# Optimization experiments

Hardware: AMD Instinct MI355X
Metric: run time of the kernel (lower is better)

Reference implementation:

```python
import jax, jax.numpy as jnp
import numpy as np

N_EMBD = 1024
N_HEAD = 16
HEAD_DIM = N_EMBD // N_HEAD


def setup_inputs() -> dict:
    key = jax.random.key(0)
    kx, kq, kk, kv, ko = jax.random.split(key, 5)
    B, T, C = 2, 2048, N_EMBD
    s = 1.0 / np.sqrt(C)
    return {
        "x": jax.random.normal(kx, (B, T, C), dtype=jnp.float32),
        "Wq": jax.random.normal(kq, (C, C), dtype=jnp.float32) * s,
        "Wk": jax.random.normal(kk, (C, C), dtype=jnp.float32) * s,
        "Wv": jax.random.normal(kv, (C, C), dtype=jnp.float32) * s,
        "Wo": jax.random.normal(ko, (C, C), dtype=jnp.float32) * s,
    }


def reference(x, Wq, Wk, Wv, Wo):
    B, T, C = x.shape
    H, D = N_HEAD, HEAD_DIM
    # projections (torch Linear: y = x @ W^T)
    q = (x @ Wq.T).reshape(B, T, H, D).transpose(0, 2, 1, 3)  # [B,H,T,D]
    k = (x @ Wk.T).reshape(B, T, H, D).transpose(0, 2, 1, 3)
    v = (x @ Wv.T).reshape(B, T, H, D).transpose(0, 2, 1, 3)
    scale = 1.0 / np.sqrt(D).astype(np.float32)
    scores = jnp.einsum("bhqd,bhkd->bhqk", q, k) * scale  # [B,H,T,T]
    causal = jnp.tril(jnp.ones((T, T), dtype=bool))
    scores = jnp.where(causal, scores, -jnp.inf)
    attn = jax.nn.softmax(scores, axis=-1)
    y = jnp.einsum("bhqk,bhkd->bhqd", attn, v)  # [B,H,T,D]
    y = y.transpose(0, 2, 1, 3).reshape(B, T, C)
    return y @ Wo.T
```

## Files before the change

### kernel.cpp

```cpp
#include <hip/hip_runtime.h>
#include <hip/hip_bf16.h>
#include <math.h>

#define SEQ   2048
#define CDIM  1024
#define NH    16
#define HD    64

#define K_SCALE 0.1803368801111204f

typedef __attribute__((ext_vector_type(8))) short bf16x8;
typedef __attribute__((ext_vector_type(4))) float f32x4;
typedef __attribute__((ext_vector_type(4))) short short4v;

__device__ __forceinline__ short f2bf(float f) {
  return (short)__builtin_bit_cast(unsigned short, __float2bfloat16(f));
}

__device__ __forceinline__ void glds16(const short* g, short* l) {
  __builtin_amdgcn_global_load_lds(
      (const __attribute__((address_space(1))) unsigned int*)g,
      (__attribute__((address_space(3))) unsigned int*)l, 16, 0, 0);
}

__global__ void cvt_all(const float* __restrict__ x,
                        const float* __restrict__ w0, const float* __restrict__ w1,
                        const float* __restrict__ w2, const float* __restrict__ w3,
                        short* __restrict__ xb,
                        short* __restrict__ d0, short* __restrict__ d1,
                        short* __restrict__ d2, short* __restrict__ d3) {
  const int y = blockIdx.y;
  const float* src;
  short* dst;
  float mult = 1.0f;
  int i = blockIdx.x * blockDim.x + threadIdx.x;
  if (y < 4) {
    src = (y == 0) ? w0 : (y == 1) ? w1 : (y == 2) ? w2 : w3;
    dst = (y == 0) ? d0 : (y == 1) ? d1 : (y == 2) ? d2 : d3;
    if (y == 1) mult = K_SCALE;
  } else {
    src = x;
    dst = xb;
    i += (y - 4) * 262144;
  }
  float4 v = reinterpret_cast<const float4*>(src)[i];
  short4v o;
  o.x = f2bf(v.x * mult); o.y = f2bf(v.y * mult);
  o.z = f2bf(v.z * mult); o.w = f2bf(v.w * mult);
  reinterpret_cast<short4v*>(dst)[i] = o;
}

template<int MODE, int BN>
__global__ __launch_bounds__(256)
void gemm_bt(const short* __restrict__ A,
             const short* __restrict__ W0, const short* __restrict__ W1, const short* __restrict__ W2,
             short* __restrict__ ob0, short* __restrict__ ob1, short* __restrict__ ob2,
             float* __restrict__ of)
{
  constexpr int K = CDIM;
  constexpr int NJF = BN / 32;
  const int z = (MODE == 0) ? blockIdx.z : 0;
  const short* W;
  short* outb = nullptr;
  if (MODE == 0) {
    W    = (z == 0) ? W0  : (z == 1) ? W1  : W2;
    outb = (z == 0) ? ob0 : (z == 1) ? ob1 : ob2;
  } else {
    W = W0;
  }
  const int m0 = blockIdx.y * 128;
  const int n0 = blockIdx.x * BN;

  __shared__ __align__(16) short As[128 * 32];
  __shared__ __align__(16) short Bs[BN * 32];

  const int tid  = threadIdx.x;
  const int lane = tid & 63;
  const int wid  = tid >> 6;
  const int wr   = wid >> 1;
  const int wc   = wid & 1;
  const int rl   = lane & 15;
  const int g    = lane >> 4;

  f32x4 acc[4][NJF];
#pragma unroll
  for (int i = 0; i < 4; ++i)
#pragma unroll
    for (int j = 0; j < NJF; ++j)
      acc[i][j] = (f32x4){0.f, 0.f, 0.f, 0.f};

  const int lrow = lane >> 2;
  const int lcol = (lane & 3) * 8;
  const int arow = wid * 32 + lrow;

  for (int kt = 0; kt < K / 32; ++kt) {
    const int k0 = kt * 32;
    glds16(&A[(size_t)(m0 + arow) * K + k0 + lcol],      &As[(wid * 32) * 32]);
    glds16(&A[(size_t)(m0 + arow + 16) * K + k0 + lcol], &As[(wid * 32 + 16) * 32]);
    if constexpr (BN == 128) {
      glds16(&W[(size_t)(n0 + arow) * K + k0 + lcol],      &Bs[(wid * 32) * 32]);
      glds16(&W[(size_t)(n0 + arow + 16) * K + k0 + lcol], &Bs[(wid * 32 + 16) * 32]);
    } else {
      glds16(&W[(size_t)(n0 + wid * 16 + lrow) * K + k0 + lcol], &Bs[(wid * 16) * 32]);
    }
    __syncthreads();

    bf16x8 af[4], bfr[NJF];
#pragma unroll
    for (int mi = 0; mi < 4; ++mi)
      af[mi] = *(const bf16x8*)&As[(wr * 64 + mi * 16 + rl) * 32 + g * 8];
#pragma unroll
    for (int nj = 0; nj < NJF; ++nj)
      bfr[nj] = *(const bf16x8*)&Bs[(wc * (BN / 2) + nj * 16 + rl) * 32 + g * 8];
#pragma unroll
    for (int mi = 0; mi < 4; ++mi)
#pragma unroll
      for (int nj = 0; nj < NJF; ++nj)
        acc[mi][nj] = __builtin_amdgcn_mfma_f32_16x16x32_bf16(af[mi], bfr[nj], acc[mi][nj], 0, 0, 0);
    __syncthreads();
  }

#pragma unroll
  for (int mi = 0; mi < 4; ++mi) {
#pragma unroll
    for (int nj = 0; nj < NJF; ++nj) {
      const int gmb = m0 + wr * 64 + mi * 16 + g * 4;
      const int gn  = n0 + wc * (BN / 2) + nj * 16 + rl;
      if (MODE == 0 && z == 2) {
        short4v pk;
#pragma unroll
        for (int r = 0; r < 4; ++r) pk[r] = f2bf(acc[mi][nj][r]);
        const int b = gmb >> 11, t = gmb & 2047;
        const int h = gn >> 6,  d = gn & 63;
        *(short4v*)&outb[(((size_t)(b * NH + h)) * HD + d) * SEQ + t] = pk;
      } else {
#pragma unroll
        for (int r = 0; r < 4; ++r) {
          const int gm = gmb + r;
          const float val = acc[mi][nj][r];
          if (MODE == 0) {
            const int b = gm >> 11, t = gm & 2047;
            const int h = gn >> 6,  d = gn & 63;
            outb[(((size_t)(b * NH + h)) * SEQ + t) * HD + d] = f2bf(val);
          } else {
            of[(size_t)gm * CDIM + gn] = val;
          }
        }
      }
    }
  }
}

__global__ __launch_bounds__(256)
void attn_kernel(const short* __restrict__ q, const short* __restrict__ k,
                 const short* __restrict__ vt, short* __restrict__ yb)
{
  const int bh  = blockIdx.y;
  const int pp  = blockIdx.x;
  const int jA  = pp;
  const int jB  = 31 - pp;
  const int tid = threadIdx.x;
  const int lane = tid & 63;
  const int wid  = tid >> 6;
  const int rl   = lane & 15;
  const int g    = lane >> 4;

  const short* Qp = q  + (size_t)bh * SEQ * HD;
  const short* Kp = k  + (size_t)bh * SEQ * HD;
  const short* Vp = vt + (size_t)bh * HD * SEQ;

  __shared__ short Ks[64 * 72];
  __shared__ short Vs[64 * 72];
  __shared__ short Ps[4][2][16 * 72];

  const int q0A = jA * 64 + wid * 16;
  const int q0B = jB * 64 + wid * 16;

  bf16x8 qfA[2], qfB[2];
#pragma unroll
  for (int ds = 0; ds < 2; ++ds) {
    qfA[ds] = *(const bf16x8*)&Qp[(size_t)(q0A + rl) * HD + ds * 32 + g * 8];
    qfB[ds] = *(const bf16x8*)&Qp[(size_t)(q0B + rl) * HD + ds * 32 + g * 8];
  }

  const short one_bf = (short)0x3F80;
  const bf16x8 onesv = (bf16x8){one_bf, one_bf, one_bf, one_bf,
                                one_bf, one_bf, one_bf, one_bf};

  f32x4 accA[4], accB[4], lAcc, lBcc;
#pragma unroll
  for (int nt = 0; nt < 4; ++nt) { accA[nt] = (f32x4){0,0,0,0}; accB[nt] = (f32x4){0,0,0,0}; }
  lAcc = (f32x4){0,0,0,0}; lBcc = (f32x4){0,0,0,0};

  const int srow = tid >> 3;
  const int scol = (tid & 7) * 8;

  auto process = [&](bf16x8 (&qf)[2], f32x4 (&acc)[4], f32x4& acc_l,
                     bool diag, int t, int q0w, short* PsW) {
    f32x4 s_[4];
#pragma unroll
    for (int ct = 0; ct < 4; ++ct) s_[ct] = (f32x4){0, 0, 0, 0};
    __builtin_amdgcn_s_setprio(1);
#pragma unroll
    for (int ct = 0; ct < 4; ++ct)
#pragma unroll
      for (int ds = 0; ds < 2; ++ds) {
        bf16x8 kf = *(const bf16x8*)&Ks[(ct * 16 + rl) * 72 + ds * 32 + g * 8];
        s_[ct] = __builtin_amdgcn_mfma_f32_16x16x32_bf16(qf[ds], kf, s_[ct], 0, 0, 0);
      }
    __builtin_amdgcn_s_setprio(0);

#pragma unroll
    for (int ct = 0; ct < 4; ++ct) {
      const int c = ct * 16 + rl;
#pragma unroll
      for (int r = 0; r < 4; ++r) {
        float sv = s_[ct][r];
        if (diag) {
          const int key = t * 64 + ct * 16 + rl;
          const int qq  = q0w + g * 4 + r;
          sv = (key <= qq) ? sv : -INFINITY;
        }
        const float p = exp2f(sv);
        PsW[(g * 4 + r) * 72 + c] = f2bf(p);
      }
    }

    __builtin_amdgcn_s_setprio(1);
#pragma unroll
    for (int ks = 0; ks < 2; ++ks) {
      bf16x8 pf = *(const bf16x8*)&PsW[rl * 72 + ks * 32 + g * 8];
      acc_l = __builtin_amdgcn_mfma_f32_16x16x32_bf16(pf, onesv, acc_l, 0, 0, 0);
#pragma unroll
      for (int nt = 0; nt < 4; ++nt) {
        bf16x8 vf = *(const bf16x8*)&Vs[(nt * 16 + rl) * 72 + ks * 32 + g * 8];
        acc[nt] = __builtin_amdgcn_mfma_f32_16x16x32_bf16(pf, vf, acc[nt], 0, 0, 0);
      }
    }
    __builtin_amdgcn_s_setprio(0);
  };

  auto epilogue = [&](f32x4 (&acc)[4], f32x4& acc_l, int q0w) {
    const int b = bh >> 4, h = bh & 15;
#pragma unroll
    for (int r = 0; r < 4; ++r) {
      const float inv = 1.0f / acc_l[r];
      const int qq = q0w + g * 4 + r;
#pragma unroll
      for (int nt = 0; nt < 4; ++nt)
        yb[((size_t)b * SEQ + qq) * CDIM + h * HD + nt * 16 + rl] = f2bf(acc[nt][r] * inv);
    }
  };

  bf16x8 k0 = *(const bf16x8*)&Kp[(size_t)srow * HD + scol];
  bf16x8 k1 = *(const bf16x8*)&Kp[(size_t)(srow + 32) * HD + scol];
  bf16x8 v0 = *(const bf16x8*)&Vp[(size_t)srow * SEQ + scol];
  bf16x8 v1 = *(const bf16x8*)&Vp[(size_t)(srow + 32) * SEQ + scol];

  for (int t = 0; t <= jB; ++t) {
    __syncthreads();
    *(bf16x8*)&Ks[srow * 72 + scol]        = k0;
    *(bf16x8*)&Ks[(srow + 32) * 72 + scol] = k1;
    *(bf16x8*)&Vs[srow * 72 + scol]        = v0;
    *(bf16x8*)&Vs[(srow + 32) * 72 + scol] = v1;
    __syncthreads();

    if (t < jB) {
      const int kn = (t + 1) * 64;
      k0 = *(const bf16x8*)&Kp[(size_t)(kn + srow) * HD + scol];
      k1 = *(const bf16x8*)&Kp[(size_t)(kn + srow + 32) * HD + scol];
      v0 = *(const bf16x8*)&Vp[(size_t)srow * SEQ + kn + scol];
      v1 = *(const bf16x8*)&Vp[(size_t)(srow + 32) * SEQ + kn + scol];
    }

    process(qfB, accB, lBcc, t == jB, t, q0B, &Ps[wid][0][0]);
    if (t <= jA)
      process(qfA, accA, lAcc, t == jA, t, q0A, &Ps[wid][1][0]);
  }

  epilogue(accB, lBcc, q0B);
  epilogue(accA, lAcc, q0A);
}

extern "C" void kernel_launch(void* const* d_in, const int* in_sizes, int n_in,
                              void* d_out, int out_size, void* d_ws, size_t ws_size,
                              hipStream_t stream) {
  const float* x  = (const float*)d_in[0];
  const float* Wq = (const float*)d_in[1];
  const float* Wk = (const float*)d_in[2];
  const float* Wv = (const float*)d_in[3];
  const float* Wo = (const float*)d_in[4];
  float* out = (float*)d_out;

  char* ws = (char*)d_ws;
  short* xb  = (short*)(ws);
  short* Wqb = (short*)(ws + ((size_t)8  << 20));
  short* Wkb = (short*)(ws + ((size_t)10 << 20));
  short* Wvb = (short*)(ws + ((size_t)12 << 20));
  short* Wob = (short*)(ws + ((size_t)14 << 20));
  short* qb  = (short*)(ws + ((size_t)16 << 20));
  short* kbp = (short*)(ws + ((size_t)24 << 20));
  short* vtp = (short*)(ws + ((size_t)32 << 20));
  short* yb  = (short*)(ws + ((size_t)40 << 20));

  cvt_all<<<dim3(1024, 8), 256, 0, stream>>>(x, Wq, Wk, Wv, Wo,
                                             xb, Wqb, Wkb, Wvb, Wob);

  gemm_bt<0, 128><<<dim3(8, 32, 3), 256, 0, stream>>>(xb, Wqb, Wkb, Wvb, qb, kbp, vtp, nullptr);

  attn_kernel<<<dim3(16, 32), 256, 0, stream>>>(qb, kbp, vtp, yb);

  gemm_bt<1, 64><<<dim3(16, 32, 1), 256, 0, stream>>>(yb, Wob, nullptr, nullptr,
                                                      nullptr, nullptr, nullptr, out);
}
```

Measured before the change: 118.0 us.

## Double-buffer K/V tiles via direct global-to-LDS loads with XOR swizzle

Replaces the register-staged K/V tile loads with async global_load_lds DMA into two LDS buffers. The next tile is prefetched while the current one is processed, which drops one __syncthreads per iteration and the VGPR round trip. The padded 72-stride layout becomes an unpadded 64-stride layout with an XOR chunk swizzle to avoid bank conflicts. This relies on the barrier waiting for the outstanding DMA loads, and it doubles the K/V LDS footprint.

```diff
diff --git a/kernel.cpp b/kernel.cpp
--- a/kernel.cpp
+++ b/kernel.cpp
@@ -169,8 +169,8 @@
   const short* Kp = k  + (size_t)bh * SEQ * HD;
   const short* Vp = vt + (size_t)bh * HD * SEQ;
 
-  __shared__ short Ks[64 * 72];
-  __shared__ short Vs[64 * 72];
+  __shared__ __align__(16) short Ks[2][64 * 64];
+  __shared__ __align__(16) short Vs[2][64 * 64];
   __shared__ short Ps[4][2][16 * 72];
 
   const int q0A = jA * 64 + wid * 16;
@@ -192,11 +192,22 @@
   for (int nt = 0; nt < 4; ++nt) { accA[nt] = (f32x4){0,0,0,0}; accB[nt] = (f32x4){0,0,0,0}; }
   lAcc = (f32x4){0,0,0,0}; lBcc = (f32x4){0,0,0,0};
 
-  const int srow = tid >> 3;
-  const int scol = (tid & 7) * 8;
+  const int lrow8  = lane >> 3;
+  const int lchunk = (lane & 7) ^ lrow8;
+  const int rx     = rl & 7;
+
+  auto stage = [&](int tile, int buf) {
+#pragma unroll
+    for (int c = 0; c < 2; ++c) {
+      const int r0 = wid * 16 + c * 8;
+      glds16(&Kp[(size_t)(tile * 64 + r0 + lrow8) * HD + lchunk * 8], &Ks[buf][r0 * 64]);
+      glds16(&Vp[(size_t)(r0 + lrow8) * SEQ + tile * 64 + lchunk * 8], &Vs[buf][r0 * 64]);
+    }
+  };
 
   auto process = [&](bf16x8 (&qf)[2], f32x4 (&acc)[4], f32x4& acc_l,
-                     bool diag, int t, int q0w, short* PsW) {
+                     bool diag, int t, int q0w, short* PsW,
+                     const short* KsB, const short* VsB) {
     f32x4 s_[4];
 #pragma unroll
     for (int ct = 0; ct < 4; ++ct) s_[ct] = (f32x4){0, 0, 0, 0};
@@ -205,7 +216,7 @@
     for (int ct = 0; ct < 4; ++ct)
 #pragma unroll
       for (int ds = 0; ds < 2; ++ds) {
-        bf16x8 kf = *(const bf16x8*)&Ks[(ct * 16 + rl) * 72 + ds * 32 + g * 8];
+        bf16x8 kf = *(const bf16x8*)&KsB[(ct * 16 + rl) * 64 + ((ds * 4 + g) ^ rx) * 8];
         s_[ct] = __builtin_amdgcn_mfma_f32_16x16x32_bf16(qf[ds], kf, s_[ct], 0, 0, 0);
       }
     __builtin_amdgcn_s_setprio(0);
@@ -233,7 +244,7 @@
       acc_l = __builtin_amdgcn_mfma_f32_16x16x32_bf16(pf, onesv, acc_l, 0, 0, 0);
 #pragma unroll
       for (int nt = 0; nt < 4; ++nt) {
-        bf16x8 vf = *(const bf16x8*)&Vs[(nt * 16 + rl) * 72 + ks * 32 + g * 8];
+        bf16x8 vf = *(const bf16x8*)&VsB[(nt * 16 + rl) * 64 + ((ks * 4 + g) ^ rx) * 8];
         acc[nt] = __builtin_amdgcn_mfma_f32_16x16x32_bf16(pf, vf, acc[nt], 0, 0, 0);
       }
     }
@@ -252,30 +263,18 @@
     }
   };
 
-  bf16x8 k0 = *(const bf16x8*)&Kp[(size_t)srow * HD + scol];
-  bf16x8 k1 = *(const bf16x8*)&Kp[(size_t)(srow + 32) * HD + scol];
-  bf16x8 v0 = *(const bf16x8*)&Vp[(size_t)srow * SEQ + scol];
-  bf16x8 v1 = *(const bf16x8*)&Vp[(size_t)(srow + 32) * SEQ + scol];
+  stage(0, 0);
 
   for (int t = 0; t <= jB; ++t) {
+    const int cb = t & 1;
     __syncthreads();
-    *(bf16x8*)&Ks[srow * 72 + scol]        = k0;
-    *(bf16x8*)&Ks[(srow + 32) * 72 + scol] = k1;
-    *(bf16x8*)&Vs[srow * 72 + scol]        = v0;
-    *(bf16x8*)&Vs[(srow + 32) * 72 + scol] = v1;
-    __syncthreads();
-
-    if (t < jB) {
-      const int kn = (t + 1) * 64;
-      k0 = *(const bf16x8*)&Kp[(size_t)(kn + srow) * HD + scol];
-      k1 = *(const bf16x8*)&Kp[(size_t)(kn + srow + 32) * HD + scol];
-      v0 = *(const bf16x8*)&Vp[(size_t)srow * SEQ + kn + scol];
-      v1 = *(const bf16x8*)&Vp[(size_t)(srow + 32) * SEQ + kn + scol];
-    }
-
-    process(qfB, accB, lBcc, t == jB, t, q0B, &Ps[wid][0][0]);
+
+    if (t < jB)
+      stage(t + 1, cb ^ 1);
+
+    process(qfB, accB, lBcc, t == jB, t, q0B, &Ps[wid][0][0], &Ks[cb][0], &Vs[cb][0]);
     if (t <= jA)
-      process(qfA, accA, lAcc, t == jA, t, q0A, &Ps[wid][1][0]);
+      process(qfA, accA, lAcc, t == jA, t, q0A, &Ps[wid][1][0], &Ks[cb][0], &Vs[cb][0]);
   }
 
   epilogue(accB, lBcc, q0B);
```

Measured after the change: 120.5 us. 2.0% more time.
